# Performance work log

Hardware: AMD Instinct MI355X
Metric: run time of the kernel (lower is better)

Reference implementation:

```python
import jax, jax.numpy as jnp
import numpy as np

B, T, C, H, E, K = 4, 2048, 512, 2048, 8, 2


def setup_inputs() -> dict:
    key = jax.random.key(0)
    ks = jax.random.split(key, 7)
    s_r = 1.0 / np.sqrt(C)
    s_h = 1.0 / np.sqrt(H)
    return {
        "x": jax.random.normal(ks[0], (B, T, C), dtype=jnp.float32),
        "Wr": jax.random.uniform(ks[1], (C, E), jnp.float32, -s_r, s_r),
        "br": jax.random.uniform(ks[2], (E,), jnp.float32, -s_r, s_r),
        "W1": jax.random.uniform(ks[3], (E, C, H), jnp.float32, -s_r, s_r),
        "b1": jax.random.uniform(ks[4], (E, H), jnp.float32, -s_r, s_r),
        "W2": jax.random.uniform(ks[5], (E, H, C), jnp.float32, -s_h, s_h),
        "b2": jax.random.uniform(ks[6], (E, C), jnp.float32, -s_h, s_h),
    }


def reference(x, Wr, br, W1, b1, W2, b2):
    # Router logits [B,T,E]
    logits = jnp.einsum("btc,ce->bte", x, Wr) + br
    topk_vals, topk_idx = jax.lax.top_k(logits, K)  # [B,T,K]
    scores = jax.nn.softmax(topk_vals, axis=-1)  # softmax over the K selected
    # Combine weights per expert: gate[b,t,e] = sum_k scores[b,t,k]*(idx==e)
    onehot = jax.nn.one_hot(topk_idx, E, dtype=x.dtype)  # [B,T,K,E]
    gate = jnp.einsum("btk,btke->bte", scores, onehot)  # [B,T,E]
    # Dense-masked expert MLPs (tokens not routed to e have gate==0)
    h = jax.nn.relu(jnp.einsum("btc,ech->bteh", x, W1) + b1)  # [B,T,E,H]
    y = jnp.einsum("bteh,ehc->btec", h, W2) + b2  # [B,T,E,C]
    out = jnp.einsum("btec,bte->btc", y, gate)  # weighted combine
    return logits, topk_idx, out
```

## Files before the change

### kernel.cpp

```cpp
#include <hip/hip_runtime.h>
#include <hip/hip_bf16.h>

#define NTOK 8192
#define NASN 16384
#define C_ 512
#define H_ 2048
#define E_ 8
#define RBC 2048
#define G1BLK 1088

typedef __bf16 bf16x8 __attribute__((ext_vector_type(8)));
typedef float f32x4 __attribute__((ext_vector_type(4)));

#define WS_COUNTS 0
#define WS_OFFS   65536
#define WS_T1S    65792
#define WS_INFO   66048
#define WS_TOKL   (WS_INFO + NTOK*16)
#define WS_SLOTS  (WS_TOKL + NASN*4)
#define WS_XBF    (WS_SLOTS + NTOK*8)
#define WS_W1B    (WS_XBF + (size_t)NTOK*C_*2)
#define WS_W2B    (WS_W1B + (size_t)E_*H_*C_*2)
#define WS_HS     (WS_W2B + (size_t)E_*H_*C_*2)
#define WS_YS     WS_XBF

__device__ __forceinline__ unsigned int f2bf(float f) {
  __hip_bfloat16 h = __float2bfloat16(f);
  return (unsigned int)*(unsigned short*)&h;
}
__device__ __forceinline__ float bf2f(unsigned int u) {
  return __int_as_float((u & 0xffffu) << 16);
}

__device__ __forceinline__ void g2l16(const unsigned short* g, unsigned short* l) {
  __builtin_amdgcn_global_load_lds(
      (const __attribute__((address_space(1))) unsigned int*)g,
      (__attribute__((address_space(3))) unsigned int*)l, 16, 0, 0);
}

__device__ __forceinline__ void stage_decode(int L, int& brow, int& q) {
  int s = L >> 3, slot = L & 7;
  int v = slot ^ (s & 7);
  brow = 2*s + (v >> 2);
  q = v & 3;
}

__global__ __launch_bounds__(256) void k_fused(
    const float* __restrict__ x, const float* __restrict__ Wr,
    const float* __restrict__ br, float* __restrict__ out_logits,
    float* __restrict__ out_idx, int4* __restrict__ info,
    int* __restrict__ counts, unsigned short* __restrict__ Xbf,
    const float* __restrict__ W1, unsigned short* __restrict__ W1b)
{
  __shared__ float tileS[128][33];
  __shared__ int bc[8];
  int b = blockIdx.x;
  int tid = threadIdx.x;

  if (b < RBC) {
    float* wls = (float*)tileS;
    if (tid < 8) bc[tid] = 0;
    #pragma unroll
    for (int it = 0; it < 4; it++) {
      int g = it*1024 + tid*4;
      float4 v = *(const float4*)(Wr + g);
      int ch = g >> 6, off = g & 63;
      float* d = wls + ch*65 + off;
      d[0] = v.x; d[1] = v.y; d[2] = v.z; d[3] = v.w;
    }
    __syncthreads();
    int t = b * 4 + (tid >> 6);
    int lane = tid & 63;
    const float4* xr = (const float4*)(x + (size_t)t * C_);
    float4 x0 = xr[lane*2], x1 = xr[lane*2+1];
    uint4 pk;
    pk.x = f2bf(x0.x) | (f2bf(x0.y) << 16);
    pk.y = f2bf(x0.z) | (f2bf(x0.w) << 16);
    pk.z = f2bf(x1.x) | (f2bf(x1.y) << 16);
    pk.w = f2bf(x1.z) | (f2bf(x1.w) << 16);
    *(uint4*)(Xbf + (size_t)t * C_ + lane*8) = pk;

    float xs[8] = {x0.x,x0.y,x0.z,x0.w,x1.x,x1.y,x1.z,x1.w};
    float acc[8] = {0,0,0,0,0,0,0,0};
    const float* wch = wls + lane*65;
    #pragma unroll
    for (int j = 0; j < 8; j++) {
      #pragma unroll
      for (int e = 0; e < 8; e++) acc[e] += xs[j] * wch[j*8 + e];
    }
    #pragma unroll
    for (int off = 1; off < 64; off <<= 1) {
      #pragma unroll
      for (int e = 0; e < 8; e++) acc[e] += __shfl_xor(acc[e], off, 64);
    }
    #pragma unroll
    for (int e = 0; e < 8; e++) acc[e] += br[e];
    if (lane == 0) {
      #pragma unroll
      for (int e = 0; e < 8; e++) out_logits[t*8 + e] = acc[e];
      int i0 = 0; float v0 = acc[0];
      #pragma unroll
      for (int e = 1; e < 8; e++) if (acc[e] > v0) { v0 = acc[e]; i0 = e; }
      int i1 = -1; float v1 = -1e30f;
      #pragma unroll
      for (int e = 0; e < 8; e++) if (e != i0 && acc[e] > v1) { v1 = acc[e]; i1 = e; }
      float d = expf(v1 - v0);
      float s1 = d / (1.0f + d);
      float s0 = 1.0f - s1;
      out_idx[t*2]     = (float)i0;
      out_idx[t*2 + 1] = (float)i1;
      info[t] = make_int4(i0, i1, __float_as_int(s0), __float_as_int(s1));
      atomicAdd(&bc[i0], 1);
      atomicAdd(&bc[i1], 1);
    }
    __syncthreads();
    if (tid < 8) counts[b*8 + tid] = bc[tid];
    return;
  }

  int bb = b - RBC;
  const float* in = W1; unsigned short* outp = W1b;
  int R = C_, S = H_;
  int bx = bb & 63, by = (bb >> 6) & 3, bz = bb >> 8;
  size_t zo = (size_t)bz * R * S;
  in += zo; outp += zo;
  int r0 = by * 128, s0 = bx * 32;
  #pragma unroll
  for (int i = 0; i < 4; i++) {
    int lin = i*256 + tid;
    int rr = lin >> 3, sq = lin & 7;
    float4 v = *(const float4*)(in + (size_t)(r0 + rr) * S + s0 + sq*4);
    tileS[rr][sq*4+0] = v.x;
    tileS[rr][sq*4+1] = v.y;
    tileS[rr][sq*4+2] = v.z;
    tileS[rr][sq*4+3] = v.w;
  }
  __syncthreads();
  #pragma unroll
  for (int i = 0; i < 4; i++) {
    int lin = i*256 + tid;
    int ss = lin >> 5, rq = lin & 31;
    ushort4 v;
    v.x = (unsigned short)f2bf(tileS[rq*4+0][ss]);
    v.y = (unsigned short)f2bf(tileS[rq*4+1][ss]);
    v.z = (unsigned short)f2bf(tileS[rq*4+2][ss]);
    v.w = (unsigned short)f2bf(tileS[rq*4+3][ss]);
    *(ushort4*)(outp + (size_t)(s0 + ss) * R + r0 + rq*4) = v;
  }
}

__global__ __launch_bounds__(256) void k_prefscatter(
    const int* __restrict__ counts, const int4* __restrict__ info,
    int* __restrict__ tokl, int2* __restrict__ slots2,
    int* __restrict__ offs, int* __restrict__ t1s)
{
  __shared__ int full_s[8][32];
  __shared__ int part_s[8][32];
  __shared__ int tot_s[8];
  __shared__ int off_s[9];
  __shared__ int cur[8];
  int c = blockIdx.x, t = threadIdx.x;
  int e = t & 7, g = t >> 3;
  int lim = c * 16;
  int full = 0, part = 0;
  for (int i = 0; i < 64; i++) {
    int rb = g*64 + i;
    int v = counts[rb*8 + e];
    full += v;
    if (rb < lim) part += v;
  }
  full_s[e][g] = full; part_s[e][g] = part;
  __syncthreads();
  if (t < 8) {
    int s = 0;
    #pragma unroll
    for (int gg = 0; gg < 32; gg++) s += full_s[t][gg];
    tot_s[t] = s;
  }
  __syncthreads();
  if (t == 0) {
    int o = 0;
    off_s[0] = 0;
    for (int ee = 0; ee < 8; ee++) { o += tot_s[ee]; off_s[ee+1] = o; }
    if (c == 0) {
      offs[0] = 0; t1s[0] = 0;
      int tt = 0;
      for (int ee = 0; ee < 8; ee++) {
        offs[ee+1] = off_s[ee+1];
        tt += (tot_s[ee] + 127) >> 7;
        t1s[ee+1] = tt;
      }
    }
  }
  __syncthreads();
  if (t < 8) {
    int mg = c >> 2;
    int bse = off_s[t];
    #pragma unroll
    for (int gg = 0; gg < 32; gg++) if (gg < mg) bse += full_s[t][gg];
    bse += part_s[t][mg];
    cur[t] = bse;
  }
  __syncthreads();
  if (t < 64) {
    int tok = c*64 + t;
    int4 nfo = info[tok];
    int r0 = atomicAdd(&cur[nfo.x], 1);
    int r1 = atomicAdd(&cur[nfo.y], 1);
    tokl[r0] = tok;
    tokl[r1] = tok;
    slots2[tok] = make_int2(r0, r1);
  }
}

__global__ __launch_bounds__(512) void k_gemm1(
    const unsigned short* __restrict__ Xbf, const int* __restrict__ tokl,
    const unsigned short* __restrict__ W1b,
    const float* __restrict__ b1, unsigned short* __restrict__ Hs,
    const int* __restrict__ offs, const int* __restrict__ t1s,
    const float* __restrict__ W2, unsigned short* __restrict__ W2b)
{
  __shared__ __align__(16) unsigned short AB[3*12288];
  int b = blockIdx.x;
  int tid = threadIdx.x;

  if (b >= G1BLK) {
    float* tS = (float*)AB;
    int b2 = b - G1BLK;
    int bx = b2 & 7, by = (b2 >> 3) & 15, bz = b2 >> 7;
    const float* in = W2 + (size_t)bz * H_ * C_;
    unsigned short* outp = W2b + (size_t)bz * H_ * C_;
    int r0 = by * 128, s0 = bx * 64;
    #pragma unroll
    for (int i = 0; i < 4; i++) {
      int lin = i*512 + tid;
      int rr = lin >> 4, cq = lin & 15;
      float4 v = *(const float4*)(in + (size_t)(r0 + rr) * C_ + s0 + cq*4);
      tS[rr*65 + cq*4+0] = v.x;
      tS[rr*65 + cq*4+1] = v.y;
      tS[rr*65 + cq*4+2] = v.z;
      tS[rr*65 + cq*4+3] = v.w;
    }
    __syncthreads();
    #pragma unroll
    for (int i = 0; i < 4; i++) {
      int lin = i*512 + tid;
      int ss = lin >> 5, rq = lin & 31;
      ushort4 v;
      v.x = (unsigned short)f2bf(tS[(rq*4+0)*65 + ss]);
      v.y = (unsigned short)f2bf(tS[(rq*4+1)*65 + ss]);
      v.z = (unsigned short)f2bf(tS[(rq*4+2)*65 + ss]);
      v.w = (unsigned short)f2bf(tS[(rq*4+3)*65 + ss]);
      *(ushort4*)(outp + (size_t)(s0 + ss) * H_ + r0 + rq*4) = v;
    }
    return;
  }

  int mo = b >> 6, rr = b & 63;
  int n0 = (rr >> 3) * 256;
  int mt = mo*8 + (rr & 7);
  if (mt >= t1s[8]) return;
  int e = 0;
  #pragma unroll
  for (int i = 0; i < 7; i++) if (mt >= t1s[i+1]) e++;
  int row0 = offs[e] + (mt - t1s[e]) * 128;
  int rowEnd = offs[e+1];
  int lane = tid & 63, w = tid >> 6;
  int wm = (w >> 2) * 64, wn = (w & 3) * 64;
  int quad = lane >> 4, l16 = lane & 15;
  const f32x4 zero = {0.f, 0.f, 0.f, 0.f};
  f32x4 acc[4][4];
  #pragma unroll
  for (int i = 0; i < 4; i++)
    #pragma unroll
    for (int j = 0; j < 4; j++) acc[i][j] = zero;
  const unsigned short* Bsrc = W1b + ((size_t)e * H_ + n0) * C_;

  const unsigned short* ga; int lao;
  const unsigned short* gb[2]; int lbo[2];
  {
    int L = w*64 + lane;
    int brow, q; stage_decode(L, brow, q);
    int gr = row0 + brow; gr = gr < NASN-1 ? gr : NASN-1;
    int trow = tokl[gr];
    ga = Xbf + (size_t)trow * C_ + q*8;
    lao = w*512;
  }
  #pragma unroll
  for (int j = 0; j < 2; j++) {
    int L = (w*2 + j)*64 + lane;
    int brow, q; stage_decode(L, brow, q);
    gb[j] = Bsrc + (size_t)brow * C_ + q*8;
    lbo[j] = 4096 + (w*2 + j)*512;
  }
  int rbase = (l16>>1)*64 + ((((l16&1)<<2) + quad) ^ (l16>>1))*8;
  const int KI = C_ / 32;

  g2l16(ga, AB + lao);
  g2l16(gb[0], AB + lbo[0]); g2l16(gb[1], AB + lbo[1]);
  g2l16(ga + 32, AB + 12288 + lao);
  g2l16(gb[0] + 32, AB + 12288 + lbo[0]); g2l16(gb[1] + 32, AB + 12288 + lbo[1]);

  {
    int cOff = 0, sOff = 2*12288;
    for (int ki = 0; ki < KI; ki++) {
      if (ki + 1 < KI)
        asm volatile("s_waitcnt vmcnt(3)" ::: "memory");
      else
        asm volatile("s_waitcnt vmcnt(0)" ::: "memory");
      asm volatile("s_barrier" ::: "memory");
      if (ki + 2 < KI) {
        int off_ = (ki + 2) * 32;
        unsigned short* nb_ = AB + sOff;
        g2l16(ga + off_, nb_ + lao);
        g2l16(gb[0] + off_, nb_ + lbo[0]);
        g2l16(gb[1] + off_, nb_ + lbo[1]);
      }
      const unsigned short* Ap_ = AB + cOff;
      const unsigned short* Bp_ = Ap_ + 4096;
      bf16x8 af_[4], bf_[4];
      #pragma unroll
      for (int i = 0; i < 4; i++)
        af_[i] = *(const bf16x8*)&Ap_[wm*32 + i*512 + rbase];
      #pragma unroll
      for (int j = 0; j < 4; j++)
        bf_[j] = *(const bf16x8*)&Bp_[wn*32 + j*512 + rbase];
      __builtin_amdgcn_s_setprio(1);
      #pragma unroll
      for (int i = 0; i < 4; i++)
        #pragma unroll
        for (int j = 0; j < 2; j++)
          acc[i][j] = __builtin_amdgcn_mfma_f32_16x16x32_bf16(af_[i], bf_[j], acc[i][j], 0, 0, 0);
      __builtin_amdgcn_s_setprio(0);
      __builtin_amdgcn_s_setprio(1);
      #pragma unroll
      for (int i = 0; i < 4; i++)
        #pragma unroll
        for (int j = 2; j < 4; j++)
          acc[i][j] = __builtin_amdgcn_mfma_f32_16x16x32_bf16(af_[i], bf_[j], acc[i][j], 0, 0, 0);
      __builtin_amdgcn_s_setprio(0);
      asm volatile("s_waitcnt lgkmcnt(0)" ::: "memory");
      cOff += 12288; if (cOff == 3*12288) cOff = 0;
      sOff += 12288; if (sOff == 3*12288) sOff = 0;
    }
  }
  __syncthreads();

  unsigned short* Lt = AB + w*4096;
  #pragma unroll
  for (int j = 0; j < 4; j++) {
    int n = n0 + wn + j*16 + l16;
    float bias = b1[e * H_ + n];
    #pragma unroll
    for (int i = 0; i < 4; i++)
      #pragma unroll
      for (int r = 0; r < 4; r++) {
        float v = acc[i][j][r] + bias;
        Lt[(i*16 + quad*4 + r)*64 + j*16 + l16] = (unsigned short)f2bf(v > 0.f ? v : 0.f);
      }
  }
  #pragma unroll
  for (int it = 0; it < 8; it++) {
    int rloc = it*8 + (lane >> 3);
    int m = row0 + wm + rloc;
    uint4 vv = *(uint4*)&Lt[rloc*64 + (lane & 7)*8];
    if (m < rowEnd)
      *(uint4*)(Hs + (size_t)m * H_ + n0 + wn + (lane & 7)*8) = vv;
  }
}

#define KLOOP(KI)                                                              \
  {                                                                            \
    int cOff = 0, sOff = 2*8192;                                               \
    for (int ki = 0; ki < (KI); ki++) {                                        \
      if (ki + 1 < (KI))                                                       \
        asm volatile("s_waitcnt vmcnt(2)" ::: "memory");                       \
      else                                                                     \
        asm volatile("s_waitcnt vmcnt(0)" ::: "memory");                       \
      asm volatile("s_barrier" ::: "memory");                                  \
      if (ki + 2 < (KI)) {                                                     \
        int off_ = (ki + 2) * 32;                                              \
        unsigned short* nb_ = AB + sOff;                                       \
        g2l16(ga + off_, nb_ + lao);                                           \
        g2l16(gb + off_, nb_ + lbo);                                           \
      }                                                                        \
      const unsigned short* Ap_ = AB + cOff;                                   \
      const unsigned short* Bp_ = Ap_ + 4096;                                  \
      bf16x8 af0 = *(const bf16x8*)&Ap_[wm*32 + 0*512 + rbase];                \
      bf16x8 af1 = *(const bf16x8*)&Ap_[wm*32 + 1*512 + rbase];                \
      bf16x8 bf0 = *(const bf16x8*)&Bp_[wn*32 + 0*512 + rbase];                \
      bf16x8 bf1 = *(const bf16x8*)&Bp_[wn*32 + 1*512 + rbase];                \
      __builtin_amdgcn_s_setprio(1);                                           \
      acc[0][0] = __builtin_amdgcn_mfma_f32_16x16x32_bf16(af0, bf0, acc[0][0], 0, 0, 0); \
      acc[0][1] = __builtin_amdgcn_mfma_f32_16x16x32_bf16(af0, bf1, acc[0][1], 0, 0, 0); \
      acc[1][0] = __builtin_amdgcn_mfma_f32_16x16x32_bf16(af1, bf0, acc[1][0], 0, 0, 0); \
      acc[1][1] = __builtin_amdgcn_mfma_f32_16x16x32_bf16(af1, bf1, acc[1][1], 0, 0, 0); \
      __builtin_amdgcn_s_setprio(0);                                           \
      bf16x8 af2 = *(const bf16x8*)&Ap_[wm*32 + 2*512 + rbase];                \
      bf16x8 af3 = *(const bf16x8*)&Ap_[wm*32 + 3*512 + rbase];                \
      __builtin_amdgcn_s_setprio(1);                                           \
      acc[2][0] = __builtin_amdgcn_mfma_f32_16x16x32_bf16(af2, bf0, acc[2][0], 0, 0, 0); \
      acc[2][1] = __builtin_amdgcn_mfma_f32_16x16x32_bf16(af2, bf1, acc[2][1], 0, 0, 0); \
      acc[3][0] = __builtin_amdgcn_mfma_f32_16x16x32_bf16(af3, bf0, acc[3][0], 0, 0, 0); \
      acc[3][1] = __builtin_amdgcn_mfma_f32_16x16x32_bf16(af3, bf1, acc[3][1], 0, 0, 0); \
      __builtin_amdgcn_s_setprio(0);                                           \
      asm volatile("s_waitcnt lgkmcnt(0)" ::: "memory");                       \
      cOff += 8192; if (cOff == 3*8192) cOff = 0;                              \
      sOff += 8192; if (sOff == 3*8192) sOff = 0;                              \
    }                                                                          \
  }

__global__ __launch_bounds__(512) void k_gemm2(
    const unsigned short* __restrict__ Hs, const unsigned short* __restrict__ W2b,
    const float* __restrict__ b2, unsigned short* __restrict__ Ys,
    const int* __restrict__ offs, const int* __restrict__ t1s)
{
  __shared__ __align__(16) unsigned short AB[3*8192];
  int b = blockIdx.x;
  int mo = b >> 5, rr = b & 31;
  int n0 = (rr >> 3) * 128;
  int mt = mo*8 + (rr & 7);
  if (mt >= t1s[8]) return;
  int e = 0;
  #pragma unroll
  for (int i = 0; i < 7; i++) if (mt >= t1s[e+1]) e++;
  int row0 = offs[e] + (mt - t1s[e]) * 128;
  int rowEnd = offs[e+1];
  int tid = threadIdx.x, lane = tid & 63, w = tid >> 6;
  int wm = (w >> 2) * 64, wn = (w & 3) * 32;
  int quad = lane >> 4, l16 = lane & 15;
  const f32x4 zero = {0.f, 0.f, 0.f, 0.f};
  f32x4 acc[4][2];
  #pragma unroll
  for (int i = 0; i < 4; i++)
    #pragma unroll
    for (int j = 0; j < 2; j++) acc[i][j] = zero;
  const unsigned short* Bsrc = W2b + ((size_t)e * C_ + n0) * H_;

  const unsigned short* ga; const unsigned short* gb;
  int lao, lbo;
  {
    int L = w*64 + lane;
    int brow, q; stage_decode(L, brow, q);
    int gr = row0 + brow; gr = gr < NASN-1 ? gr : NASN-1;
    ga = Hs + (size_t)gr * H_ + q*8;
    gb = Bsrc + (size_t)brow * H_ + q*8;
    lao = w*512;
    lbo = 4096 + w*512;
  }
  int rbase = (l16>>1)*64 + ((((l16&1)<<2) + quad) ^ (l16>>1))*8;
  const int KI = H_ / 32;

  g2l16(ga, AB + lao);            g2l16(gb, AB + lbo);
  g2l16(ga + 32, AB + 8192 + lao); g2l16(gb + 32, AB + 8192 + lbo);

  KLOOP(KI);
  __syncthreads();

  unsigned short* Lt = AB + w*2048;
  #pragma unroll
  for (int j = 0; j < 2; j++) {
    int n = n0 + wn + j*16 + l16;
    float bias = b2[e * C_ + n];
    #pragma unroll
    for (int i = 0; i < 4; i++)
      #pragma unroll
      for (int r = 0; r < 4; r++)
        Lt[(i*16 + quad*4 + r)*32 + j*16 + l16] =
            (unsigned short)f2bf(acc[i][j][r] + bias);
  }
  #pragma unroll
  for (int it = 0; it < 4; it++) {
    int rloc = it*16 + (lane >> 2);
    int m = row0 + wm + rloc;
    uint4 vv = *(uint4*)&Lt[rloc*32 + (lane & 3)*8];
    if (m < rowEnd)
      *(uint4*)(Ys + (size_t)m * C_ + n0 + wn + (lane & 3)*8) = vv;
  }
}

__global__ __launch_bounds__(256) void k_combine(
    const unsigned short* __restrict__ Ys, const int4* __restrict__ info,
    const int2* __restrict__ slots2, float* __restrict__ outp)
{
  int t = blockIdx.x * 4 + (threadIdx.x >> 6);
  int lane = threadIdx.x & 63;
  int4 nfo = info[t];
  int2 ss = slots2[t];
  float g0 = __int_as_float(nfo.z), g1 = __int_as_float(nfo.w);
  uint4 a = *(const uint4*)(Ys + (size_t)ss.x * C_ + lane*8);
  uint4 bb = *(const uint4*)(Ys + (size_t)ss.y * C_ + lane*8);
  unsigned int au[4] = {a.x, a.y, a.z, a.w};
  unsigned int bu[4] = {bb.x, bb.y, bb.z, bb.w};
  float vals[8];
  #pragma unroll
  for (int q = 0; q < 4; q++) {
    vals[q*2]   = g0*bf2f(au[q])       + g1*bf2f(bu[q]);
    vals[q*2+1] = g0*bf2f(au[q] >> 16) + g1*bf2f(bu[q] >> 16);
  }
  float4 o0, o1;
  o0.x = vals[0]; o0.y = vals[1]; o0.z = vals[2]; o0.w = vals[3];
  o1.x = vals[4]; o1.y = vals[5]; o1.z = vals[6]; o1.w = vals[7];
  float4* o = (float4*)(outp + (size_t)t * C_ + lane*8);
  o[0] = o0;
  o[1] = o1;
}

extern "C" void kernel_launch(void* const* d_in, const int* in_sizes, int n_in,
                              void* d_out, int out_size, void* d_ws, size_t ws_size,
                              hipStream_t stream)
{
  const float* x  = (const float*)d_in[0];
  const float* Wr = (const float*)d_in[1];
  const float* br = (const float*)d_in[2];
  const float* W1 = (const float*)d_in[3];
  const float* b1 = (const float*)d_in[4];
  const float* W2 = (const float*)d_in[5];
  const float* b2 = (const float*)d_in[6];
  float* out = (float*)d_out;
  char* ws = (char*)d_ws;

  int*  counts = (int*)(ws + WS_COUNTS);
  int*  offs   = (int*)(ws + WS_OFFS);
  int*  t1s    = (int*)(ws + WS_T1S);
  int4* info   = (int4*)(ws + WS_INFO);
  int*  tokl   = (int*)(ws + WS_TOKL);
  int2* slots2 = (int2*)(ws + WS_SLOTS);
  unsigned short* Xbf = (unsigned short*)(ws + WS_XBF);
  unsigned short* W1b = (unsigned short*)(ws + WS_W1B);
  unsigned short* W2b = (unsigned short*)(ws + WS_W2B);
  unsigned short* Hs  = (unsigned short*)(ws + WS_HS);
  unsigned short* Ys  = (unsigned short*)(ws + WS_YS);

  k_fused<<<2*RBC, 256, 0, stream>>>(x, Wr, br, out, out + 65536, info,
                                     counts, Xbf, W1, W1b);
  k_prefscatter<<<128, 256, 0, stream>>>(counts, info, tokl, slots2, offs, t1s);
  k_gemm1<<<G1BLK + 1024, 512, 0, stream>>>(Xbf, tokl, W1b, b1, Hs, offs, t1s,
                                            W2, W2b);
  k_gemm2<<<17*32, 512, 0, stream>>>(Hs, W2b, b2, Ys, offs, t1s);
  k_combine<<<NTOK/4, 256, 0, stream>>>(Ys, info, slots2, out + 81920);
}
```

Measured before the change: 245.1 us.

## Enlarge gemm1 tile to 256x256 with 8x4 MFMA accumulators per wave

Raises the grouped GEMM1 M-tile from 128 to 256 rows, adding a separate 256-row tile prefix (t2s) and cutting the block count. Each wave now computes 128x64 outputs with 32 accumulators, which reuses each loaded W1 tile across twice as many tokens. LDS grows to 96KB per block and register pressure roughly doubles, which can lower occupancy and increase padding waste for experts with few tokens.

```diff
diff --git a/kernel.cpp b/kernel.cpp
--- a/kernel.cpp
+++ b/kernel.cpp
@@ -7,7 +7,7 @@
 #define H_ 2048
 #define E_ 8
 #define RBC 2048
-#define G1BLK 1088
+#define G1BLK 576
 
 typedef __bf16 bf16x8 __attribute__((ext_vector_type(8)));
 typedef float f32x4 __attribute__((ext_vector_type(4)));
@@ -15,6 +15,7 @@
 #define WS_COUNTS 0
 #define WS_OFFS   65536
 #define WS_T1S    65792
+#define WS_T2S    65856
 #define WS_INFO   66048
 #define WS_TOKL   (WS_INFO + NTOK*16)
 #define WS_SLOTS  (WS_TOKL + NASN*4)
@@ -152,7 +153,7 @@
 __global__ __launch_bounds__(256) void k_prefscatter(
     const int* __restrict__ counts, const int4* __restrict__ info,
     int* __restrict__ tokl, int2* __restrict__ slots2,
-    int* __restrict__ offs, int* __restrict__ t1s)
+    int* __restrict__ offs, int* __restrict__ t1s, int* __restrict__ t2s)
 {
   __shared__ int full_s[8][32];
   __shared__ int part_s[8][32];
@@ -183,12 +184,14 @@
     off_s[0] = 0;
     for (int ee = 0; ee < 8; ee++) { o += tot_s[ee]; off_s[ee+1] = o; }
     if (c == 0) {
-      offs[0] = 0; t1s[0] = 0;
-      int tt = 0;
+      offs[0] = 0; t1s[0] = 0; t2s[0] = 0;
+      int tt = 0, tt2 = 0;
       for (int ee = 0; ee < 8; ee++) {
         offs[ee+1] = off_s[ee+1];
         tt += (tot_s[ee] + 127) >> 7;
         t1s[ee+1] = tt;
+        tt2 += (tot_s[ee] + 255) >> 8;
+        t2s[ee+1] = tt2;
       }
     }
   }
@@ -217,10 +220,10 @@
     const unsigned short* __restrict__ Xbf, const int* __restrict__ tokl,
     const unsigned short* __restrict__ W1b,
     const float* __restrict__ b1, unsigned short* __restrict__ Hs,
-    const int* __restrict__ offs, const int* __restrict__ t1s,
+    const int* __restrict__ offs, const int* __restrict__ t2s,
     const float* __restrict__ W2, unsigned short* __restrict__ W2b)
 {
-  __shared__ __align__(16) unsigned short AB[3*12288];
+  __shared__ __align__(16) unsigned short AB[3*16384];
   int b = blockIdx.x;
   int tid = threadIdx.x;
 
@@ -259,113 +262,119 @@
   int mo = b >> 6, rr = b & 63;
   int n0 = (rr >> 3) * 256;
   int mt = mo*8 + (rr & 7);
-  if (mt >= t1s[8]) return;
+  if (mt >= t2s[8]) return;
   int e = 0;
   #pragma unroll
-  for (int i = 0; i < 7; i++) if (mt >= t1s[i+1]) e++;
-  int row0 = offs[e] + (mt - t1s[e]) * 128;
+  for (int i = 0; i < 7; i++) if (mt >= t2s[i+1]) e++;
+  int row0 = offs[e] + (mt - t2s[e]) * 256;
   int rowEnd = offs[e+1];
   int lane = tid & 63, w = tid >> 6;
-  int wm = (w >> 2) * 64, wn = (w & 3) * 64;
+  int wr = w >> 2, wc = w & 3;
   int quad = lane >> 4, l16 = lane & 15;
   const f32x4 zero = {0.f, 0.f, 0.f, 0.f};
-  f32x4 acc[4][4];
-  #pragma unroll
-  for (int i = 0; i < 4; i++)
+  f32x4 acc[8][4];
+  #pragma unroll
+  for (int i = 0; i < 8; i++)
     #pragma unroll
     for (int j = 0; j < 4; j++) acc[i][j] = zero;
   const unsigned short* Bsrc = W1b + ((size_t)e * H_ + n0) * C_;
 
-  const unsigned short* ga; int lao;
-  const unsigned short* gb[2]; int lbo[2];
-  {
-    int L = w*64 + lane;
+  const unsigned short* gaA[2]; const unsigned short* gbB[2];
+  #pragma unroll
+  for (int r = 0; r < 2; r++) {
+    int L = r*512 + tid;
     int brow, q; stage_decode(L, brow, q);
     int gr = row0 + brow; gr = gr < NASN-1 ? gr : NASN-1;
     int trow = tokl[gr];
-    ga = Xbf + (size_t)trow * C_ + q*8;
-    lao = w*512;
-  }
-  #pragma unroll
-  for (int j = 0; j < 2; j++) {
-    int L = (w*2 + j)*64 + lane;
+    gaA[r] = Xbf + (size_t)trow * C_ + q*8;
+  }
+  #pragma unroll
+  for (int r = 0; r < 2; r++) {
+    int L = r*512 + tid;
     int brow, q; stage_decode(L, brow, q);
-    gb[j] = Bsrc + (size_t)brow * C_ + q*8;
-    lbo[j] = 4096 + (w*2 + j)*512;
-  }
+    gbB[r] = Bsrc + (size_t)brow * C_ + q*8;
+  }
+  int aBase0 = w*512, aBase1 = 4096 + w*512;
+  int bBase0 = 8192 + w*512, bBase1 = 12288 + w*512;
   int rbase = (l16>>1)*64 + ((((l16&1)<<2) + quad) ^ (l16>>1))*8;
   const int KI = C_ / 32;
 
-  g2l16(ga, AB + lao);
-  g2l16(gb[0], AB + lbo[0]); g2l16(gb[1], AB + lbo[1]);
-  g2l16(ga + 32, AB + 12288 + lao);
-  g2l16(gb[0] + 32, AB + 12288 + lbo[0]); g2l16(gb[1] + 32, AB + 12288 + lbo[1]);
+  g2l16(gaA[0], AB + aBase0);            g2l16(gaA[1], AB + aBase1);
+  g2l16(gbB[0], AB + bBase0);            g2l16(gbB[1], AB + bBase1);
+  g2l16(gaA[0] + 32, AB + 16384 + aBase0); g2l16(gaA[1] + 32, AB + 16384 + aBase1);
+  g2l16(gbB[0] + 32, AB + 16384 + bBase0); g2l16(gbB[1] + 32, AB + 16384 + bBase1);
 
   {
-    int cOff = 0, sOff = 2*12288;
+    int cOff = 0, sOff = 2*16384;
     for (int ki = 0; ki < KI; ki++) {
       if (ki + 1 < KI)
-        asm volatile("s_waitcnt vmcnt(3)" ::: "memory");
+        asm volatile("s_waitcnt vmcnt(4)" ::: "memory");
       else
         asm volatile("s_waitcnt vmcnt(0)" ::: "memory");
       asm volatile("s_barrier" ::: "memory");
       if (ki + 2 < KI) {
         int off_ = (ki + 2) * 32;
         unsigned short* nb_ = AB + sOff;
-        g2l16(ga + off_, nb_ + lao);
-        g2l16(gb[0] + off_, nb_ + lbo[0]);
-        g2l16(gb[1] + off_, nb_ + lbo[1]);
+        g2l16(gaA[0] + off_, nb_ + aBase0);
+        g2l16(gaA[1] + off_, nb_ + aBase1);
+        g2l16(gbB[0] + off_, nb_ + bBase0);
+        g2l16(gbB[1] + off_, nb_ + bBase1);
       }
       const unsigned short* Ap_ = AB + cOff;
-      const unsigned short* Bp_ = Ap_ + 4096;
-      bf16x8 af_[4], bf_[4];
-      #pragma unroll
-      for (int i = 0; i < 4; i++)
-        af_[i] = *(const bf16x8*)&Ap_[wm*32 + i*512 + rbase];
+      const unsigned short* Bp_ = Ap_ + 8192;
+      bf16x8 af_[8], bf_[4];
+      #pragma unroll
+      for (int i = 0; i < 8; i++)
+        af_[i] = *(const bf16x8*)&Ap_[wr*4096 + i*512 + rbase];
       #pragma unroll
       for (int j = 0; j < 4; j++)
-        bf_[j] = *(const bf16x8*)&Bp_[wn*32 + j*512 + rbase];
+        bf_[j] = *(const bf16x8*)&Bp_[wc*2048 + j*512 + rbase];
       __builtin_amdgcn_s_setprio(1);
       #pragma unroll
       for (int i = 0; i < 4; i++)
         #pragma unroll
-        for (int j = 0; j < 2; j++)
+        for (int j = 0; j < 4; j++)
           acc[i][j] = __builtin_amdgcn_mfma_f32_16x16x32_bf16(af_[i], bf_[j], acc[i][j], 0, 0, 0);
       __builtin_amdgcn_s_setprio(0);
       __builtin_amdgcn_s_setprio(1);
       #pragma unroll
-      for (int i = 0; i < 4; i++)
+      for (int i = 4; i < 8; i++)
         #pragma unroll
-        for (int j = 2; j < 4; j++)
+        for (int j = 0; j < 4; j++)
           acc[i][j] = __builtin_amdgcn_mfma_f32_16x16x32_bf16(af_[i], bf_[j], acc[i][j], 0, 0, 0);
       __builtin_amdgcn_s_setprio(0);
       asm volatile("s_waitcnt lgkmcnt(0)" ::: "memory");
-      cOff += 12288; if (cOff == 3*12288) cOff = 0;
-      sOff += 12288; if (sOff == 3*12288) sOff = 0;
+      cOff += 16384; if (cOff == 3*16384) cOff = 0;
+      sOff += 16384; if (sOff == 3*16384) sOff = 0;
     }
   }
   __syncthreads();
 
   unsigned short* Lt = AB + w*4096;
   #pragma unroll
-  for (int j = 0; j < 4; j++) {
-    int n = n0 + wn + j*16 + l16;
-    float bias = b1[e * H_ + n];
-    #pragma unroll
-    for (int i = 0; i < 4; i++)
-      #pragma unroll
-      for (int r = 0; r < 4; r++) {
-        float v = acc[i][j][r] + bias;
-        Lt[(i*16 + quad*4 + r)*64 + j*16 + l16] = (unsigned short)f2bf(v > 0.f ? v : 0.f);
+  for (int p = 0; p < 2; p++) {
+    #pragma unroll
+    for (int j = 0; j < 4; j++) {
+      int n = n0 + wc*64 + j*16 + l16;
+      float bias = b1[e * H_ + n];
+      #pragma unroll
+      for (int i2 = 0; i2 < 4; i2++) {
+        int i = p*4 + i2;
+        #pragma unroll
+        for (int r = 0; r < 4; r++) {
+          float v = acc[i][j][r] + bias;
+          Lt[(i2*16 + quad*4 + r)*64 + j*16 + l16] = (unsigned short)f2bf(v > 0.f ? v : 0.f);
+        }
       }
-  }
-  #pragma unroll
-  for (int it = 0; it < 8; it++) {
-    int rloc = it*8 + (lane >> 3);
-    int m = row0 + wm + rloc;
-    uint4 vv = *(uint4*)&Lt[rloc*64 + (lane & 7)*8];
-    if (m < rowEnd)
-      *(uint4*)(Hs + (size_t)m * H_ + n0 + wn + (lane & 7)*8) = vv;
+    }
+    #pragma unroll
+    for (int it = 0; it < 8; it++) {
+      int rloc = it*8 + (lane >> 3);
+      int m = row0 + wr*128 + p*64 + rloc;
+      uint4 vv = *(uint4*)&Lt[rloc*64 + (lane & 7)*8];
+      if (m < rowEnd)
+        *(uint4*)(Hs + (size_t)m * H_ + n0 + wc*64 + (lane & 7)*8) = vv;
+    }
   }
 }
 
@@ -523,6 +532,7 @@
   int*  counts = (int*)(ws + WS_COUNTS);
   int*  offs   = (int*)(ws + WS_OFFS);
   int*  t1s    = (int*)(ws + WS_T1S);
+  int*  t2s    = (int*)(ws + WS_T2S);
   int4* info   = (int4*)(ws + WS_INFO);
   int*  tokl   = (int*)(ws + WS_TOKL);
   int2* slots2 = (int2*)(ws + WS_SLOTS);
@@ -534,8 +544,8 @@
 
   k_fused<<<2*RBC, 256, 0, stream>>>(x, Wr, br, out, out + 65536, info,
                                      counts, Xbf, W1, W1b);
-  k_prefscatter<<<128, 256, 0, stream>>>(counts, info, tokl, slots2, offs, t1s);
-  k_gemm1<<<G1BLK + 1024, 512, 0, stream>>>(Xbf, tokl, W1b, b1, Hs, offs, t1s,
+  k_prefscatter<<<128, 256, 0, stream>>>(counts, info, tokl, slots2, offs, t1s, t2s);
+  k_gemm1<<<G1BLK + 1024, 512, 0, stream>>>(Xbf, tokl, W1b, b1, Hs, offs, t2s,
                                             W2, W2b);
   k_gemm2<<<17*32, 512, 0, stream>>>(Hs, W2b, b2, Ys, offs, t1s);
   k_combine<<<NTOK/4, 256, 0, stream>>>(Ys, info, slots2, out + 81920);
```

After: 251.8 us. +2.7%, slower.
